# Kernel tuning notes

Hardware: AMD Instinct MI355X
Metric: run time of the kernel (lower is better)

## Reference

```python
import jax, jax.numpy as jnp
import numpy as np

N_NODES = 50000
N_EDGES = 800000
N_GRAPHS = 128
EMBED = 256
OUT = 128
LAYERS = 5
ATOM_COLS, ATOM_VOCAB = 9, 128
BOND_COLS, BOND_VOCAB = 3, 8
EPS = 1e-5


def setup_inputs() -> dict:
    key = jax.random.key(0)
    ks = jax.random.split(key, 16)
    nfeat = jax.random.randint(ks[0], (N_NODES, ATOM_COLS), 0, ATOM_VOCAB)
    efeat = jax.random.randint(ks[1], (N_EDGES, BOND_COLS), 0, BOND_VOCAB)
    src = jax.random.randint(ks[2], (N_EDGES,), 0, N_NODES)
    dst = jax.random.randint(ks[3], (N_EDGES,), 0, N_NODES)
    graph_ids = jnp.sort(jax.random.randint(ks[4], (N_NODES,), 0, N_GRAPHS))
    s = 0.02
    atom_emb = jax.random.normal(ks[5], (ATOM_COLS, ATOM_VOCAB, EMBED), jnp.float32) * s
    edge_emb = jax.random.normal(ks[6], (LAYERS, BOND_COLS, BOND_VOCAB, EMBED), jnp.float32) * s
    W = jax.random.normal(ks[7], (LAYERS, EMBED, EMBED), jnp.float32) * (1.0 / np.sqrt(EMBED))
    b = jnp.zeros((LAYERS, EMBED), jnp.float32)
    gamma = jnp.ones((LAYERS, EMBED), jnp.float32)
    beta = jnp.zeros((LAYERS, EMBED), jnp.float32)
    Wp = jax.random.normal(ks[8], (EMBED, OUT), jnp.float32) * (1.0 / np.sqrt(EMBED))
    bp = jnp.zeros((OUT,), jnp.float32)
    return {"nfeat": nfeat, "efeat": efeat, "src": src, "dst": dst,
            "graph_ids": graph_ids, "atom_emb": atom_emb, "edge_emb": edge_emb,
            "W": W, "b": b, "gamma": gamma, "beta": beta, "Wp": Wp, "bp": bp}


def _gcn_forward(nfeat, efeat, src, dst, graph_ids,
                 atom_emb, edge_emb, W, b, gamma, beta, Wp, bp):
    # atom encoder: sum embeddings over categorical columns -> [N, D]
    h = jnp.zeros((N_NODES, EMBED), jnp.float32)
    for c in range(ATOM_COLS):
        h = h + atom_emb[c][nfeat[:, c]]

    # in-degree + 1 (DGL in_degrees counts incoming edges at dst)
    degs = jax.ops.segment_sum(jnp.ones((N_EDGES,), jnp.float32), dst,
                               num_segments=N_NODES) + 1.0  # [N]

    for l in range(LAYERS):
        # edge encoder for this layer: sum over bond columns -> [E, D]
        e = jnp.zeros((N_EDGES, EMBED), jnp.float32)
        for c in range(BOND_COLS):
            e = e + edge_emb[l, c][efeat[:, c]]
        # u_add_e message + sum reduce at destination
        msg = h[src] + e                                    # [E, D]
        neigh = jax.ops.segment_sum(msg, dst, num_segments=N_NODES)  # [N, D]
        # degree-normalize then project
        h = ((h + neigh) / degs[:, None]) @ W[l] + b[l]
        # batch norm over nodes (training statistics)
        mu = jnp.mean(h, axis=0)
        var = jnp.mean(jnp.square(h - mu), axis=0)
        h = (h - mu) * jax.lax.rsqrt(var + EPS) * gamma[l] + beta[l]
        # relu (dropout is identity at eval)
        h = jax.nn.relu(h)

    # mean pooling per graph
    sums = jax.ops.segment_sum(h, graph_ids, num_segments=N_GRAPHS)  # [G, D]
    cnts = jax.ops.segment_sum(jnp.ones((N_NODES,), jnp.float32), graph_ids,
                               num_segments=N_GRAPHS)
    g = sums / jnp.maximum(cnts, 1.0)[:, None]
    return g @ Wp + bp  # [G, OUT]


def reference(nfeat, efeat, src, dst, graph_ids, atom_emb, edge_emb,
              W, b, gamma, beta, Wp, bp):
    return _gcn_forward(nfeat, efeat, src, dst, graph_ids,
                        atom_emb, edge_emb, W, b, gamma, beta, Wp, bp)
```

## Files before the change

kernel.cpp:

```cpp
#include <hip/hip_runtime.h>

#define N_NODESC 50000
#define N_PAD 50176
#define N_EDGESC 800000
#define N_GRAPHSC 128
#define EMBEDC 256
#define MTILES 392
#define SLAB ((long)N_PAD * 32)
#define NRANGE 6272

typedef __attribute__((ext_vector_type(8))) _Float16 hf8;
typedef __attribute__((ext_vector_type(4))) float fx4;

__device__ __forceinline__ float h2f(unsigned short u) {
  _Float16 h = *(_Float16*)&u;
  return (float)h;
}
__device__ __forceinline__ unsigned short f2h(float f) {
  _Float16 h = (_Float16)f;
  return *(unsigned short*)&h;
}
__device__ __forceinline__ unsigned int packh2(float lo, float hi) {
  return (unsigned int)f2h(lo) | ((unsigned int)f2h(hi) << 16);
}

__global__ __launch_bounds__(256) void atom_encode_k(
    const int* __restrict__ nfeat, const float* __restrict__ atom_emb,
    unsigned short* __restrict__ h16)
{
  int w = threadIdx.x >> 6, lane = threadIdx.x & 63;
  int n = blockIdx.x * 4 + w;
  if (n >= N_NODESC) return;
  const int* nf = nfeat + n * 9;
  float ax = 0.f, ay = 0.f, az = 0.f, aw = 0.f;
#pragma unroll
  for (int c = 0; c < 9; ++c) {
    int idx = nf[c];
    const float4* row = (const float4*)(atom_emb + (c * 128 + idx) * EMBEDC);
    float4 v = row[lane];
    ax += v.x; ay += v.y; az += v.z; aw += v.w;
  }
  ushort4 o;
  o.x = f2h(ax); o.y = f2h(ay); o.z = f2h(az); o.w = f2h(aw);
  int col = lane * 4;
  *(ushort4*)(h16 + (long)(col >> 5) * SLAB + (long)n * 32 + (col & 31)) = o;
}

__global__ __launch_bounds__(256) void deg_k(
    const int* __restrict__ dst, int* __restrict__ degs)
{
  int e = blockIdx.x * 256 + threadIdx.x;
  if (e >= N_EDGESC) return;
  atomicAdd(&degs[dst[e]], 1);
}

__global__ __launch_bounds__(256) void scan_partial_k(
    const int* __restrict__ deg, int* __restrict__ bsum)
{
  __shared__ int buf[256];
  int b = blockIdx.x, t = threadIdx.x;
  int idx0 = b * 1024 + t * 4;
  int s = 0;
#pragma unroll
  for (int i = 0; i < 4; ++i) {
    int idx = idx0 + i;
    if (idx < N_NODESC) s += deg[idx];
  }
  buf[t] = s;
  __syncthreads();
  for (int off = 1; off < 256; off <<= 1) {
    int add = (t >= off) ? buf[t - off] : 0;
    __syncthreads();
    buf[t] += add;
    __syncthreads();
  }
  if (t == 255) bsum[b] = buf[255];
}
__global__ __launch_bounds__(64) void scan_sums_k(
    const int* __restrict__ bsum, int* __restrict__ boff)
{
  __shared__ int buf[64];
  int t = threadIdx.x;
  int v = (t < 49) ? bsum[t] : 0;
  buf[t] = v;
  __syncthreads();
  for (int off = 1; off < 64; off <<= 1) {
    int add = (t >= off) ? buf[t - off] : 0;
    __syncthreads();
    buf[t] += add;
    __syncthreads();
  }
  if (t < 49) boff[t] = buf[t] - v;
  if (t == 48) boff[49] = buf[48];
}
__global__ __launch_bounds__(256) void scan_final_k(
    const int* __restrict__ deg, const int* __restrict__ boff,
    int* __restrict__ row_start)
{
  __shared__ int buf[256];
  int b = blockIdx.x, t = threadIdx.x;
  int idx0 = b * 1024 + t * 4;
  int loc[4];
  int s = 0;
#pragma unroll
  for (int i = 0; i < 4; ++i) {
    int idx = idx0 + i;
    int v = (idx < N_NODESC) ? deg[idx] : 0;
    loc[i] = v; s += v;
  }
  buf[t] = s;
  __syncthreads();
  for (int off = 1; off < 256; off <<= 1) {
    int add = (t >= off) ? buf[t - off] : 0;
    __syncthreads();
    buf[t] += add;
    __syncthreads();
  }
  int run = boff[b] + buf[t] - s;
#pragma unroll
  for (int i = 0; i < 4; ++i) {
    int idx = idx0 + i;
    if (idx < N_NODESC) row_start[idx] = run;
    run += loc[i];
  }
  if (b == 48 && t == 255) row_start[N_NODESC] = boff[49];
}

__global__ __launch_bounds__(256) void scatter_k(
    const int* __restrict__ src, const int* __restrict__ dst,
    const int* __restrict__ row_start, int* __restrict__ fill,
    int* __restrict__ csrc, int* __restrict__ ceid)
{
  int b = blockIdx.x;
  int r = b & 7;
  int e = (b >> 3) * 256 + threadIdx.x;
  if (e >= N_EDGESC) return;
  int d = dst[e];
  int lo = r * NRANGE;
  if (d < lo || d >= lo + NRANGE) return;
  int pos = row_start[d] + atomicAdd(&fill[d], 1);
  csrc[pos] = src[e];
  ceid[pos] = e;
}

__global__ __launch_bounds__(256) void cntf_k(
    const int* __restrict__ ceid, const int* __restrict__ row_start,
    const int* __restrict__ efeat, unsigned short* __restrict__ cntf)
{
  __shared__ int lc[256 * 25];
  int t = threadIdx.x;
  int n = blockIdx.x * 256 + t;
  int base = t * 25;
#pragma unroll
  for (int j = 0; j < 24; ++j) lc[base + j] = 0;
  float inv = 0.f;
  if (n < N_NODESC) {
    int s0 = row_start[n], s1 = row_start[n + 1];
    inv = 1.0f / (float)(s1 - s0 + 1);
    for (int e = s0; e < s1; ++e) {
      int eid = ceid[e];
      int v0 = efeat[eid * 3 + 0];
      int v1 = efeat[eid * 3 + 1];
      int v2 = efeat[eid * 3 + 2];
      lc[base + v0]++;
      lc[base + 8 + v1]++;
      lc[base + 16 + v2]++;
    }
  }
  unsigned int* o = (unsigned int*)(cntf + (long)n * 32);
#pragma unroll
  for (int j = 0; j < 12; ++j)
    o[j] = packh2((float)lc[base + 2 * j] * inv, (float)lc[base + 2 * j + 1] * inv);
#pragma unroll
  for (int j = 12; j < 16; ++j) o[j] = 0u;
}

__global__ __launch_bounds__(256) void wprep_k(
    const float* __restrict__ W, unsigned short* __restrict__ Wt)
{
  int tid = blockIdx.x * 256 + threadIdx.x;
  int l = tid >> 16, r = tid & 65535;
  int n = r >> 8, k = r & 255;
  float w = W[(long)l * 65536 + k * 256 + n];
  Wt[tid] = f2h(w);
}

__global__ __launch_bounds__(256) void ew_k(
    const float* __restrict__ edge_emb, const float* __restrict__ W,
    unsigned short* __restrict__ EWt)
{
  __shared__ float e[256];
  int l = blockIdx.x / 24, j = blockIdx.x % 24;
  int c = threadIdx.x;
  e[c] = edge_emb[(long)l * 6144 + j * 256 + c];
  __syncthreads();
  const float* Wl = W + (long)l * 65536;
  float acc = 0.f;
#pragma unroll 8
  for (int k = 0; k < 256; ++k) acc += e[k] * Wl[k * 256 + c];
  EWt[((long)l * 256 + c) * 32 + j] = f2h(acc);
}

template<int FUSE_BN>
__device__ __forceinline__ hf8 bnval(const uint4 u, const hf8 scv, const hf8 shv)
{
  union { uint4 u4; hf8 h8; } cv;
  cv.u4 = u;
  hf8 y = cv.h8;
  if (FUSE_BN) {
    y = y * scv + shv;
    y = __builtin_elementwise_max(y, (hf8)0);
  }
  return y;
}

template<int FUSE_BN>
__global__ __launch_bounds__(256) void aggregate_t(
    const unsigned short* __restrict__ tab_base,
    const int* __restrict__ csrc, const int* __restrict__ row_start,
    const unsigned short* __restrict__ sc16,
    const unsigned short* __restrict__ sh16,
    unsigned short* __restrict__ X16)
{
  int bid = blockIdx.x;
  int s = bid & 7;
  int grp = bid >> 3;
  int lane = threadIdx.x & 63;
  int w = threadIdx.x >> 6;
  int nd = lane >> 3;
  int g = (lane >> 2) & 1;
  int q = lane & 3;
  int n = grp * 32 + w * 8 + nd;
  if (n >= N_NODESC) return;
  const unsigned short* tab = tab_base + (long)s * SLAB;
  hf8 scv = (hf8)0, shv = (hf8)0;
  if (FUSE_BN) {
    scv = *(const hf8*)(sc16 + s * 32 + q * 8);
    shv = *(const hf8*)(sh16 + s * 32 + q * 8);
  }
  int s0 = row_start[n], s1 = row_start[n + 1];
  hf8 hacc = (hf8)0;
  if (g == 0) {
    uint4 u = *(const uint4*)(tab + (long)n * 32 + q * 8);
    hacc = hacc + bnval<FUSE_BN>(u, scv, shv);
  }
  int e = s0 + g;
  for (; e + 2 < s1; e += 4) {
    int i0 = csrc[e];
    int i1 = csrc[e + 2];
    uint4 u0 = *(const uint4*)(tab + (long)i0 * 32 + q * 8);
    uint4 u1 = *(const uint4*)(tab + (long)i1 * 32 + q * 8);
    hacc = hacc + bnval<FUSE_BN>(u0, scv, shv);
    hacc = hacc + bnval<FUSE_BN>(u1, scv, shv);
  }
  if (e < s1) {
    int i0 = csrc[e];
    uint4 u = *(const uint4*)(tab + (long)i0 * 32 + q * 8);
    hacc = hacc + bnval<FUSE_BN>(u, scv, shv);
  }
  float a[8];
#pragma unroll
  for (int k = 0; k < 8; ++k) a[k] = (float)hacc[k];
#pragma unroll
  for (int k = 0; k < 8; ++k) a[k] += __shfl_xor(a[k], 4);
  if (g == 0) {
    float inv = 1.0f / (float)(s1 - s0 + 1);
    uint4 o;
    o.x = packh2(a[0] * inv, a[1] * inv);
    o.y = packh2(a[2] * inv, a[3] * inv);
    o.z = packh2(a[4] * inv, a[5] * inv);
    o.w = packh2(a[6] * inv, a[7] * inv);
    *(uint4*)(X16 + (long)s * SLAB + (long)n * 32 + q * 8) = o;
  }
}

__global__ __launch_bounds__(256) void gemm_k(
    const unsigned short* __restrict__ X16, const unsigned short* __restrict__ Bt,
    const unsigned short* __restrict__ cntf, const unsigned short* __restrict__ EWt,
    const float* __restrict__ bl, unsigned short* __restrict__ Y16,
    float* __restrict__ Pp)
{
  __shared__ unsigned short As[128 * 72];
  __shared__ unsigned short Bs[128 * 72];
  __shared__ float red_s[256];
  __shared__ float red_q[256];

  int t = threadIdx.x;
  int bm = blockIdx.x, bn = blockIdx.y;
  int row0 = bm * 128, nc0 = bn * 128;
  int w = t >> 6, l = t & 63;
  int wr = w >> 1, wc = w & 1;
  int lr = l & 15, lk = l >> 4;

  fx4 acc[4][4];
#pragma unroll
  for (int i = 0; i < 4; ++i)
#pragma unroll
    for (int j = 0; j < 4; ++j) acc[i][j] = (fx4){0.f, 0.f, 0.f, 0.f};

  for (int kb = 0; kb < 5; ++kb) {
    __syncthreads();
    if (kb < 4) {
      int kc = kb * 64;
#pragma unroll
      for (int q = 0; q < 2; ++q) {
        int id = q * 256 + t;
        int r = id >> 2, c16 = (id & 3) << 4;
        int ktot = kc + c16;
        long gA = (long)(ktot >> 5) * SLAB + (long)(row0 + r) * 32 + (ktot & 31);
        long gB = (long)(nc0 + r) * 256 + ktot;
        *(uint4*)&As[r * 72 + c16] = *(const uint4*)(X16 + gA);
        *(uint4*)&As[r * 72 + c16 + 8] = *(const uint4*)(X16 + gA + 8);
        *(uint4*)&Bs[r * 72 + c16] = *(const uint4*)(Bt + gB);
        *(uint4*)&Bs[r * 72 + c16 + 8] = *(const uint4*)(Bt + gB + 8);
      }
    } else {
#pragma unroll
      for (int q = 0; q < 2; ++q) {
        int id = q * 256 + t;
        int r = id >> 2, c8 = (id & 3) << 3;
        *(uint4*)&As[r * 72 + c8] = *(const uint4*)(cntf + (long)(row0 + r) * 32 + c8);
        *(uint4*)&Bs[r * 72 + c8] = *(const uint4*)(EWt + (long)(nc0 + r) * 32 + c8);
      }
    }
    __syncthreads();
    int nks = (kb < 4) ? 2 : 1;
    for (int ks = 0; ks < nks; ++ks) {
      int ko = ks * 32 + lk * 8;
      hf8 af[4], bf[4];
#pragma unroll
      for (int f = 0; f < 4; ++f) {
        af[f] = *(const hf8*)&As[(wr * 64 + f * 16 + lr) * 72 + ko];
        bf[f] = *(const hf8*)&Bs[(wc * 64 + f * 16 + lr) * 72 + ko];
      }
#pragma unroll
      for (int fm = 0; fm < 4; ++fm)
#pragma unroll
        for (int fn = 0; fn < 4; ++fn)
          acc[fm][fn] = __builtin_amdgcn_mfma_f32_16x16x32_f16(
              af[fm], bf[fn], acc[fm][fn], 0, 0, 0);
    }
  }

  float bcol[4];
#pragma unroll
  for (int fn = 0; fn < 4; ++fn) bcol[fn] = bl[nc0 + wc * 64 + fn * 16 + lr];
  float sp[4] = {0.f, 0.f, 0.f, 0.f}, qp[4] = {0.f, 0.f, 0.f, 0.f};
#pragma unroll
  for (int fm = 0; fm < 4; ++fm)
#pragma unroll
    for (int fn = 0; fn < 4; ++fn) {
      int cl = wc * 64 + fn * 16 + lr;
      int col = nc0 + cl;
      long ybase = (long)(col >> 5) * SLAB + (col & 31);
#pragma unroll
      for (int j = 0; j < 4; ++j) {
        int rl = wr * 64 + fm * 16 + lk * 4 + j;
        float v = acc[fm][fn][j] + bcol[fn];
        Y16[ybase + (long)(row0 + rl) * 32] = f2h(v);
        sp[fn] += v; qp[fn] += v * v;
      }
    }
#pragma unroll
  for (int fn = 0; fn < 4; ++fn) {
    sp[fn] += __shfl_xor(sp[fn], 16);
    sp[fn] += __shfl_xor(sp[fn], 32);
    qp[fn] += __shfl_xor(qp[fn], 16);
    qp[fn] += __shfl_xor(qp[fn], 32);
  }
  if (lk == 0) {
#pragma unroll
    for (int fn = 0; fn < 4; ++fn) {
      red_s[w * 64 + fn * 16 + lr] = sp[fn];
      red_q[w * 64 + fn * 16 + lr] = qp[fn];
    }
  }
  __syncthreads();
  if (t < 128) {
    float s = red_s[t] + red_s[128 + t];
    float q = red_q[t] + red_q[128 + t];
    float* p = Pp + (bm * 2 + bn) * 256;
    p[t] = s;
    p[128 + t] = q;
  }
}

__global__ __launch_bounds__(128) void stats_finalize_k(
    const float* __restrict__ Pp, const float* __restrict__ bl,
    const float* __restrict__ gamma, const float* __restrict__ beta,
    float* __restrict__ scale, float* __restrict__ shiftv,
    unsigned short* __restrict__ sc16, unsigned short* __restrict__ sh16)
{
  __shared__ float red_s[128];
  __shared__ float red_q[128];
  int c = blockIdx.x;
  int half = c >> 7, cl = c & 127;
  int t = threadIdx.x;
  float s = 0.f, q = 0.f;
  for (int bm = t; bm < MTILES; bm += 128) {
    const float* p = Pp + (bm * 2 + half) * 256;
    s += p[cl];
    q += p[128 + cl];
  }
  red_s[t] = s; red_q[t] = q;
  __syncthreads();
#pragma unroll
  for (int off = 64; off > 0; off >>= 1) {
    if (t < off) {
      red_s[t] += red_s[t + off];
      red_q[t] += red_q[t + off];
    }
    __syncthreads();
  }
  if (t == 0) {
    s = red_s[0]; q = red_q[0];
    float bc = bl[c];
    s -= (float)(N_PAD - N_NODESC) * bc;
    q -= (float)(N_PAD - N_NODESC) * bc * bc;
    const float invN = 1.0f / (float)N_NODESC;
    float mu = s * invN;
    float var = q * invN - mu * mu;
    float rsq = rsqrtf(var + 1e-5f);
    float sc = gamma[c] * rsq;
    float sh = beta[c] - mu * sc;
    scale[c] = sc;
    shiftv[c] = sh;
    sc16[c] = f2h(sc);
    sh16[c] = f2h(sh);
  }
}

__device__ __forceinline__ int lower_bound_g(const int* gid, int n, int g)
{
  int lo = 0, hi = n;
  while (lo < hi) {
    int mid = (lo + hi) >> 1;
    if (gid[mid] < g) lo = mid + 1; else hi = mid;
  }
  return lo;
}

__global__ __launch_bounds__(512) void pool_k(
    const unsigned short* __restrict__ Y16, const int* __restrict__ gid,
    const float* __restrict__ scale, const float* __restrict__ shiftv,
    float* __restrict__ gpool)
{
  __shared__ float red[8 * 256];
  int g = blockIdx.x;
  int lo = lower_bound_g(gid, N_NODESC, g);
  int hi = lower_bound_g(gid, N_NODESC, g + 1);
  int t = threadIdx.x;
  int w = t >> 6, lane = t & 63;
  int col = lane * 4;
  long ybase = (long)(col >> 5) * SLAB + (col & 31);
  float4 sc = *(const float4*)(scale + col);
  float4 sh = *(const float4*)(shiftv + col);
  float a0 = 0.f, a1 = 0.f, a2 = 0.f, a3 = 0.f;
  for (int r = lo + w; r < hi; r += 8) {
    ushort4 u = *(const ushort4*)(Y16 + ybase + (long)r * 32);
    a0 += fmaxf(0.f, h2f(u.x) * sc.x + sh.x);
    a1 += fmaxf(0.f, h2f(u.y) * sc.y + sh.y);
    a2 += fmaxf(0.f, h2f(u.z) * sc.z + sh.z);
    a3 += fmaxf(0.f, h2f(u.w) * sc.w + sh.w);
  }
  *(float4*)&red[w * 256 + col] = make_float4(a0, a1, a2, a3);
  __syncthreads();
  if (t < 256) {
    float s = 0.f;
#pragma unroll
    for (int j = 0; j < 8; ++j) s += red[j * 256 + t];
    int c = hi - lo;
    gpool[g * 256 + t] = s / (float)(c > 0 ? c : 1);
  }
}

__global__ __launch_bounds__(128) void final_k(
    const float* __restrict__ gpool, const float* __restrict__ Wp,
    const float* __restrict__ bp, float* __restrict__ out)
{
  __shared__ float gr[256];
  int g = blockIdx.x, t = threadIdx.x;
  gr[t] = gpool[g * 256 + t];
  gr[t + 128] = gpool[g * 256 + t + 128];
  __syncthreads();
  float acc = bp[t];
#pragma unroll 8
  for (int k = 0; k < 256; ++k) acc += gr[k] * Wp[k * 128 + t];
  out[g * 128 + t] = acc;
}

extern "C" void kernel_launch(void* const* d_in, const int* in_sizes, int n_in,
                              void* d_out, int out_size, void* d_ws, size_t ws_size,
                              hipStream_t stream)
{
  (void)in_sizes; (void)n_in; (void)out_size; (void)ws_size;
  const int* nfeat = (const int*)d_in[0];
  const int* efeat = (const int*)d_in[1];
  const int* src = (const int*)d_in[2];
  const int* dst = (const int*)d_in[3];
  const int* gid = (const int*)d_in[4];
  const float* atom_emb = (const float*)d_in[5];
  const float* edge_emb = (const float*)d_in[6];
  const float* W = (const float*)d_in[7];
  const float* b = (const float*)d_in[8];
  const float* gamma = (const float*)d_in[9];
  const float* beta = (const float*)d_in[10];
  const float* Wp = (const float*)d_in[11];
  const float* bp = (const float*)d_in[12];
  float* out = (float*)d_out;

  char* ws = (char*)d_ws;
  unsigned short* h16 = (unsigned short*)ws; ws += (size_t)N_PAD * 512;
  unsigned short* Y16 = (unsigned short*)ws; ws += (size_t)N_PAD * 512;
  unsigned short* X16 = (unsigned short*)ws; ws += (size_t)N_PAD * 512;
  unsigned short* Wt = (unsigned short*)ws; ws += 5 * 65536 * 2;
  unsigned short* EWt = (unsigned short*)ws; ws += 5 * 256 * 32 * 2;
  unsigned short* cntf = (unsigned short*)ws; ws += (size_t)N_PAD * 32 * 2;
  int* csrc = (int*)ws; ws += 3200000;
  int* ceid = (int*)ws; ws += 3200000;
  int* row_start = (int*)ws; ws += 200064;
  int* degs_i = (int*)ws; ws += 200064;
  int* fill = (int*)ws; ws += 200064;
  int* bsum = (int*)ws; ws += 256;
  int* boff = (int*)ws; ws += 256;
  float* Pp = (float*)ws; ws += MTILES * 2 * 256 * 4;
  float* scale = (float*)ws; ws += 1024;
  float* shiftv = (float*)ws; ws += 1024;
  unsigned short* sc16 = (unsigned short*)ws; ws += 512;
  unsigned short* sh16 = (unsigned short*)ws; ws += 512;
  float* gpool = (float*)ws; ws += 131072;

  hipMemsetAsync(degs_i, 0, 200000, stream);
  hipMemsetAsync(fill, 0, 200000, stream);
  for (int s = 0; s < 8; ++s)
    hipMemsetAsync(X16 + (size_t)s * SLAB + (size_t)N_NODESC * 32, 0,
                   (size_t)(N_PAD - N_NODESC) * 64, stream);

  wprep_k<<<1280, 256, 0, stream>>>(W, Wt);
  ew_k<<<120, 256, 0, stream>>>(edge_emb, W, EWt);
  atom_encode_k<<<12500, 256, 0, stream>>>(nfeat, atom_emb, h16);
  deg_k<<<3125, 256, 0, stream>>>(dst, degs_i);
  scan_partial_k<<<49, 256, 0, stream>>>(degs_i, bsum);
  scan_sums_k<<<1, 64, 0, stream>>>(bsum, boff);
  scan_final_k<<<49, 256, 0, stream>>>(degs_i, boff, row_start);
  scatter_k<<<25000, 256, 0, stream>>>(src, dst, row_start, fill, csrc, ceid);
  cntf_k<<<196, 256, 0, stream>>>(ceid, row_start, efeat, cntf);

  aggregate_t<0><<<12504, 256, 0, stream>>>(h16, csrc, row_start,
                                            nullptr, nullptr, X16);
  for (int l = 0; l < 5; ++l) {
    gemm_k<<<dim3(MTILES, 2), 256, 0, stream>>>(X16, Wt + l * 65536, cntf,
                                                EWt + l * 8192, b + l * 256,
                                                Y16, Pp);
    stats_finalize_k<<<256, 128, 0, stream>>>(Pp, b + l * 256, gamma + l * 256,
                                              beta + l * 256, scale, shiftv,
                                              sc16, sh16);
    if (l < 4)
      aggregate_t<1><<<12504, 256, 0, stream>>>(Y16, csrc, row_start,
                                                sc16, sh16, X16);
  }

  pool_k<<<128, 512, 0, stream>>>(Y16, gid, scale, shiftv, gpool);
  final_k<<<128, 128, 0, stream>>>(gpool, Wp, bp, out);
}
```

Before: 569.0 us.

## Sort nodes by in-degree for load-balanced aggregation and unroll gather loop

Builds a degree histogram, scans it, and fills a node permutation so that aggregate kernels process nodes grouped by in-degree, reducing warp divergence from uneven neighbor counts. The gather loop is also unrolled to four outstanding row loads per lane group, increasing memory-level parallelism. This adds three small preprocessing kernels. It also scatters output writes and self-row reads, since consecutive lanes now touch non-adjacent nodes.

```diff
diff --git a/kernel.cpp b/kernel.cpp
--- a/kernel.cpp
+++ b/kernel.cpp
@@ -124,6 +124,41 @@
     run += loc[i];
   }
   if (b == 48 && t == 255) row_start[N_NODESC] = boff[49];
+}
+
+__global__ __launch_bounds__(256) void dhist_k(
+    const int* __restrict__ row_start, int* __restrict__ dhist)
+{
+  int n = blockIdx.x * 256 + threadIdx.x;
+  if (n >= N_NODESC) return;
+  int d = row_start[n + 1] - row_start[n];
+  atomicAdd(&dhist[d < 63 ? d : 63], 1);
+}
+__global__ __launch_bounds__(64) void dscan_k(
+    const int* __restrict__ dhist, int* __restrict__ doff)
+{
+  __shared__ int buf[64];
+  int t = threadIdx.x;
+  int v = dhist[t];
+  buf[t] = v;
+  __syncthreads();
+  for (int off = 1; off < 64; off <<= 1) {
+    int add = (t >= off) ? buf[t - off] : 0;
+    __syncthreads();
+    buf[t] += add;
+    __syncthreads();
+  }
+  doff[t] = buf[t] - v;
+}
+__global__ __launch_bounds__(256) void dfill_k(
+    const int* __restrict__ row_start, int* __restrict__ doff,
+    int* __restrict__ nperm)
+{
+  int n = blockIdx.x * 256 + threadIdx.x;
+  if (n >= N_NODESC) return;
+  int d = row_start[n + 1] - row_start[n];
+  int pos = atomicAdd(&doff[d < 63 ? d : 63], 1);
+  nperm[pos] = n;
 }
 
 __global__ __launch_bounds__(256) void scatter_k(
@@ -218,6 +253,7 @@
 __global__ __launch_bounds__(256) void aggregate_t(
     const unsigned short* __restrict__ tab_base,
     const int* __restrict__ csrc, const int* __restrict__ row_start,
+    const int* __restrict__ nperm,
     const unsigned short* __restrict__ sc16,
     const unsigned short* __restrict__ sh16,
     unsigned short* __restrict__ X16)
@@ -230,8 +266,9 @@
   int nd = lane >> 3;
   int g = (lane >> 2) & 1;
   int q = lane & 3;
-  int n = grp * 32 + w * 8 + nd;
-  if (n >= N_NODESC) return;
+  int gidx = grp * 32 + w * 8 + nd;
+  if (gidx >= N_NODESC) return;
+  int n = nperm[gidx];
   const unsigned short* tab = tab_base + (long)s * SLAB;
   hf8 scv = (hf8)0, shv = (hf8)0;
   if (FUSE_BN) {
@@ -245,15 +282,21 @@
     hacc = hacc + bnval<FUSE_BN>(u, scv, shv);
   }
   int e = s0 + g;
-  for (; e + 2 < s1; e += 4) {
+  for (; e + 6 < s1; e += 8) {
     int i0 = csrc[e];
     int i1 = csrc[e + 2];
+    int i2 = csrc[e + 4];
+    int i3 = csrc[e + 6];
     uint4 u0 = *(const uint4*)(tab + (long)i0 * 32 + q * 8);
     uint4 u1 = *(const uint4*)(tab + (long)i1 * 32 + q * 8);
+    uint4 u2 = *(const uint4*)(tab + (long)i2 * 32 + q * 8);
+    uint4 u3 = *(const uint4*)(tab + (long)i3 * 32 + q * 8);
     hacc = hacc + bnval<FUSE_BN>(u0, scv, shv);
     hacc = hacc + bnval<FUSE_BN>(u1, scv, shv);
-  }
-  if (e < s1) {
+    hacc = hacc + bnval<FUSE_BN>(u2, scv, shv);
+    hacc = hacc + bnval<FUSE_BN>(u3, scv, shv);
+  }
+  for (; e < s1; e += 2) {
     int i0 = csrc[e];
     uint4 u = *(const uint4*)(tab + (long)i0 * 32 + q * 8);
     hacc = hacc + bnval<FUSE_BN>(u, scv, shv);
@@ -521,8 +564,11 @@
   int* row_start = (int*)ws; ws += 200064;
   int* degs_i = (int*)ws; ws += 200064;
   int* fill = (int*)ws; ws += 200064;
+  int* nperm = (int*)ws; ws += 200064;
   int* bsum = (int*)ws; ws += 256;
   int* boff = (int*)ws; ws += 256;
+  int* dhist = (int*)ws; ws += 256;
+  int* doff = (int*)ws; ws += 256;
   float* Pp = (float*)ws; ws += MTILES * 2 * 256 * 4;
   float* scale = (float*)ws; ws += 1024;
   float* shiftv = (float*)ws; ws += 1024;
@@ -532,6 +578,7 @@
 
   hipMemsetAsync(degs_i, 0, 200000, stream);
   hipMemsetAsync(fill, 0, 200000, stream);
+  hipMemsetAsync(dhist, 0, 256, stream);
   for (int s = 0; s < 8; ++s)
     hipMemsetAsync(X16 + (size_t)s * SLAB + (size_t)N_NODESC * 32, 0,
                    (size_t)(N_PAD - N_NODESC) * 64, stream);
@@ -543,10 +590,13 @@
   scan_partial_k<<<49, 256, 0, stream>>>(degs_i, bsum);
   scan_sums_k<<<1, 64, 0, stream>>>(bsum, boff);
   scan_final_k<<<49, 256, 0, stream>>>(degs_i, boff, row_start);
+  dhist_k<<<196, 256, 0, stream>>>(row_start, dhist);
+  dscan_k<<<1, 64, 0, stream>>>(dhist, doff);
+  dfill_k<<<196, 256, 0, stream>>>(row_start, doff, nperm);
   scatter_k<<<25000, 256, 0, stream>>>(src, dst, row_start, fill, csrc, ceid);
   cntf_k<<<196, 256, 0, stream>>>(ceid, row_start, efeat, cntf);
 
-  aggregate_t<0><<<12504, 256, 0, stream>>>(h16, csrc, row_start,
+  aggregate_t<0><<<12504, 256, 0, stream>>>(h16, csrc, row_start, nperm,
                                             nullptr, nullptr, X16);
   for (int l = 0; l < 5; ++l) {
     gemm_k<<<dim3(MTILES, 2), 256, 0, stream>>>(X16, Wt + l * 65536, cntf,
@@ -556,7 +606,7 @@
                                               beta + l * 256, scale, shiftv,
                                               sc16, sh16);
     if (l < 4)
-      aggregate_t<1><<<12504, 256, 0, stream>>>(Y16, csrc, row_start,
+      aggregate_t<1><<<12504, 256, 0, stream>>>(Y16, csrc, row_start, nperm,
                                                 sc16, sh16, X16);
   }
 
```

After: 870.3 us. +53.0%, slower.
